# Performance work log

Hardware: AMD Instinct MI355X
Metric: run time of the kernel (lower is better)

## Reference

```python
import jax, jax.numpy as jnp
import numpy as np

B, N, MW, H, C, K = 64, 8192, 128, 8, 1024, 3
HD = C // H  # head width = 128


def setup_inputs() -> dict:
    key = jax.random.key(0)
    ks = jax.random.split(key, 16)
    s = 0.02
    return {
        "control_state": jax.random.normal(ks[0], (B, C), jnp.float32),
        "memory": jax.random.normal(ks[1], (B, N, MW), jnp.float32),
        "prev_weights": jax.nn.softmax(jax.random.normal(ks[2], (B, H, N), jnp.float32), axis=-1),
        "defaults": jax.nn.softmax(jax.random.normal(ks[3], (B, H, N), jnp.float32), axis=-1),
        "W_head": s * jax.random.normal(ks[4], (C, H * HD), jnp.float32),
        "b_head": jnp.zeros((H, HD), jnp.float32),
        "W_reset": s * jax.random.normal(ks[5], (H, HD, 1), jnp.float32),
        "b_reset": jnp.zeros((H, 1), jnp.float32),
        "W_key": s * jax.random.normal(ks[6], (H, HD, MW), jnp.float32),
        "b_key": jnp.zeros((H, MW), jnp.float32),
        "W_beta": s * jax.random.normal(ks[7], (H, HD, 1), jnp.float32),
        "b_beta": jnp.zeros((H, 1), jnp.float32),
        "W_gate": s * jax.random.normal(ks[8], (H, HD, 1), jnp.float32),
        "b_gate": jnp.zeros((H, 1), jnp.float32),
        "W_shift": s * jax.random.normal(ks[9], (H, HD, K), jnp.float32),
        "b_shift": jnp.zeros((H, K), jnp.float32),
        "W_gamma": s * jax.random.normal(ks[10], (H, HD, 1), jnp.float32),
        "b_gamma": jnp.zeros((H, 1), jnp.float32),
        "merge_w": jax.random.normal(ks[11], (H,), jnp.float32) * 0.3 + 1.0 / H,
    }


def reference(control_state, memory, prev_weights, defaults, W_head, b_head,
              W_reset, b_reset, W_key, b_key, W_beta, b_beta, W_gate, b_gate,
              W_shift, b_shift, W_gamma, b_gamma, merge_w):
    eps = 1e-8
    # head projection: [B,C] -> [B,H,HD]
    heads = (control_state @ W_head).reshape(-1, H, HD) + b_head
    # sigmoid reset gate: convex blend of prior weights with defaults
    reset_p = jax.nn.sigmoid(jnp.einsum('bhd,hdo->bho', heads, W_reset) + b_reset)  # [B,H,1]
    weights = prev_weights * (1.0 - reset_p) + defaults * reset_p
    # NTM addressing parameters (per-head linear maps)
    key_ = jnp.einsum('bhd,hdw->bhw', heads, W_key) + b_key          # [B,H,MW]
    beta = jax.nn.softplus(jnp.einsum('bhd,hdo->bho', heads, W_beta) + b_beta)   # [B,H,1]
    gate = jax.nn.sigmoid(jnp.einsum('bhd,hdo->bho', heads, W_gate) + b_gate)    # [B,H,1]
    shift = jax.nn.softmax(jnp.einsum('bhd,hdk->bhk', heads, W_shift) + b_shift, axis=-1)  # [B,H,K]
    gamma = 1.0 + jax.nn.softplus(jnp.einsum('bhd,hdo->bho', heads, W_gamma) + b_gamma)    # [B,H,1]
    # content addressing: sharpened cosine similarity softmax over memory slots
    sim = jnp.einsum('bhw,bnw->bhn', key_, memory)
    sim = sim / (jnp.linalg.norm(key_, axis=-1, keepdims=True)
                 * jnp.linalg.norm(memory, axis=-1)[:, None, :] + eps)
    content = jax.nn.softmax(beta * sim, axis=-1)                    # [B,H,N]
    # interpolate with (possibly reset) prior weights
    w_g = gate * content + (1.0 - gate) * weights
    # location addressing: circular convolution with shift kernel symmetric around 0
    w_s = sum(shift[..., j:j + 1] * jnp.roll(w_g, j - K // 2, axis=-1) for j in range(K))
    # sharpening
    w_pow = (w_s + eps) ** gamma
    new_w = w_pow / jnp.sum(w_pow, axis=-1, keepdims=True)           # [B,H,N]
    # read: per-head attention matmul against memory, then weighted head merge
    headed = jnp.einsum('bhn,bnw->bhw', new_w, memory)               # [B,H,MW]
    out = jnp.einsum('bhw,h->bw', headed, merge_w)                   # [B,MW]
    return out, new_w
```

## Files before the change

kernel.cpp:

```cpp
#include <hip/hip_runtime.h>
#include <hip/hip_bf16.h>
#include <math.h>

#define Bb 64
#define Nn 8192
#define MWw 128
#define Hh 8
#define Cc 1024
#define HDd 128
#define Kk 3

__device__ __forceinline__ float dot4(float4 a, float4 b) {
  return a.x*b.x + a.y*b.y + a.z*b.z + a.w*b.w;
}
__device__ __forceinline__ float sigmoidf_(float x) { return 1.0f / (1.0f + __expf(-x)); }
__device__ __forceinline__ float softplusf_(float x) {
  return fmaxf(x, 0.0f) + log1pf(__expf(-fabsf(x)));
}

__global__ __launch_bounds__(1024) void k_params(
    const float* __restrict__ cs, const float* __restrict__ W_head, const float* __restrict__ b_head,
    const float* __restrict__ W_reset, const float* __restrict__ b_reset,
    const float* __restrict__ W_key, const float* __restrict__ b_key,
    const float* __restrict__ W_beta, const float* __restrict__ b_beta,
    const float* __restrict__ W_gate, const float* __restrict__ b_gate,
    const float* __restrict__ W_shift, const float* __restrict__ b_shift,
    const float* __restrict__ W_gamma, const float* __restrict__ b_gamma,
    float* __restrict__ key_ws, float* __restrict__ params)
{
  int bh = blockIdx.x;
  int b = bh >> 3, h = bh & 7;
  int t = threadIdx.x;
  int d = t & 127, sl = t >> 7;
  __shared__ float red[8][128];
  __shared__ float head_s[128];
  __shared__ float key_s[128];

  const float* csb = cs + b * Cc + sl * 128;
  const float* w0 = W_head + (size_t)(sl * 128) * (Hh * HDd) + h * HDd + d;
  float acc = 0.0f;
  #pragma unroll 8
  for (int c = 0; c < 128; ++c) acc = fmaf(csb[c], w0[(size_t)c * (Hh * HDd)], acc);
  red[sl][d] = acc;
  __syncthreads();
  if (t < 128) {
    float s = b_head[h * HDd + t];
    #pragma unroll
    for (int j = 0; j < 8; ++j) s += red[j][t];
    head_s[t] = s;
  }
  __syncthreads();

  {
    const float* wk = W_key + (size_t)h * HDd * MWw + (sl * 16) * MWw + d;
    float ka = 0.0f;
    #pragma unroll
    for (int dd = 0; dd < 16; ++dd) ka = fmaf(head_s[sl * 16 + dd], wk[dd * MWw], ka);
    red[sl][d] = ka;
  }
  __syncthreads();
  if (t < 128) {
    float kv = b_key[h * MWw + t];
    #pragma unroll
    for (int j = 0; j < 8; ++j) kv += red[j][t];
    key_ws[bh * MWw + t] = kv;
    key_s[t] = kv;
  }
  __syncthreads();

  float hd = head_s[d];
  float v;
  switch (sl) {
    case 0: v = hd * W_reset[h * HDd + d]; break;
    case 1: v = hd * W_beta[h * HDd + d]; break;
    case 2: v = hd * W_gate[h * HDd + d]; break;
    case 3: v = hd * W_gamma[h * HDd + d]; break;
    case 4: v = hd * W_shift[(h * HDd + d) * Kk + 0]; break;
    case 5: v = hd * W_shift[(h * HDd + d) * Kk + 1]; break;
    case 6: v = hd * W_shift[(h * HDd + d) * Kk + 2]; break;
    default: v = key_s[d] * key_s[d]; break;
  }
  red[sl][d] = v;
  __syncthreads();
  for (int s = 64; s > 0; s >>= 1) {
    if (d < s) red[sl][d] += red[sl][d + s];
    __syncthreads();
  }
  if (t == 0) {
    float reset = sigmoidf_(red[0][0] + b_reset[h]);
    float beta  = softplusf_(red[1][0] + b_beta[h]);
    float gate  = sigmoidf_(red[2][0] + b_gate[h]);
    float gamma = 1.0f + softplusf_(red[3][0] + b_gamma[h]);
    float a0 = red[4][0] + b_shift[h * Kk + 0];
    float a1 = red[5][0] + b_shift[h * Kk + 1];
    float a2 = red[6][0] + b_shift[h * Kk + 2];
    float mx = fmaxf(a0, fmaxf(a1, a2));
    float e0 = __expf(a0 - mx), e1 = __expf(a1 - mx), e2 = __expf(a2 - mx);
    float inv = 1.0f / (e0 + e1 + e2);
    float* P = params + bh * 8;
    P[0] = reset; P[1] = beta; P[2] = gate; P[3] = gamma;
    P[4] = e0 * inv; P[5] = e1 * inv; P[6] = e2 * inv;
    P[7] = sqrtf(red[7][0]);
  }
}

__global__ __launch_bounds__(256, 2) void k_sim(
    const float* __restrict__ mem, const float* __restrict__ key_ws,
    const float* __restrict__ params, float* __restrict__ e_ws, float* __restrict__ Z)
{
  int b = blockIdx.y, chunk = blockIdx.x;
  int t = threadIdx.x;
  int lane = t & 63, wid = t >> 6;
  int sub = lane & 7, rid = lane >> 3;
  __shared__ float4 keys[8][32];
  __shared__ float betas[8], knorms[8];
  __shared__ float e_s[8][520];
  if (t < 8) { betas[t] = params[(b * 8 + t) * 8 + 1]; knorms[t] = params[(b * 8 + t) * 8 + 7]; }
  {
    int h = t >> 5, q = t & 31;
    keys[h][q] = ((const float4*)key_ws)[(b * 8 + h) * 32 + q];
  }
  __syncthreads();

  float4 kreg[8][4];
  #pragma unroll
  for (int h2 = 0; h2 < 8; ++h2) {
    kreg[h2][0] = keys[h2][sub];
    kreg[h2][1] = keys[h2][sub + 8];
    kreg[h2][2] = keys[h2][sub + 16];
    kreg[h2][3] = keys[h2][sub + 24];
  }

  const float4* m4 = (const float4*)mem + (size_t)b * Nn * 32;
  float beta = betas[sub], kn = knorms[sub];
  float zloc = 0.0f;
  int n0 = chunk * 512;

  #pragma unroll 1
  for (int itr = 0; itr < 8; ++itr) {
    int nb = n0 + itr * 64 + wid * 16 + rid;
    float4 m[2][4];
    float nrm[2];
    float acc[2][8];
    #pragma unroll
    for (int r = 0; r < 2; ++r) {
      const float4* rp = m4 + (size_t)(nb + r * 8) * 32 + sub;
      m[r][0] = rp[0]; m[r][1] = rp[8]; m[r][2] = rp[16]; m[r][3] = rp[24];
    }
    #pragma unroll
    for (int r = 0; r < 2; ++r) {
      nrm[r] = dot4(m[r][0], m[r][0]) + dot4(m[r][1], m[r][1])
             + dot4(m[r][2], m[r][2]) + dot4(m[r][3], m[r][3]);
      #pragma unroll
      for (int h2 = 0; h2 < 8; ++h2) {
        acc[r][h2] = dot4(m[r][0], kreg[h2][0]) + dot4(m[r][1], kreg[h2][1])
                   + dot4(m[r][2], kreg[h2][2]) + dot4(m[r][3], kreg[h2][3]);
      }
    }
    #pragma unroll
    for (int r = 0; r < 2; ++r) {
      float* a = acc[r];
      bool h1 = (sub & 1) != 0;
      float v40 = (h1 ? a[1] : a[0]) + __shfl_xor(h1 ? a[0] : a[1], 1, 64);
      float v41 = (h1 ? a[3] : a[2]) + __shfl_xor(h1 ? a[2] : a[3], 1, 64);
      float v42 = (h1 ? a[5] : a[4]) + __shfl_xor(h1 ? a[4] : a[5], 1, 64);
      float v43 = (h1 ? a[7] : a[6]) + __shfl_xor(h1 ? a[6] : a[7], 1, 64);
      bool h2b = (sub & 2) != 0;
      float v20 = (h2b ? v41 : v40) + __shfl_xor(h2b ? v40 : v41, 2, 64);
      float v21 = (h2b ? v43 : v42) + __shfl_xor(h2b ? v42 : v43, 2, 64);
      bool h4 = (sub & 4) != 0;
      float dsum = (h4 ? v21 : v20) + __shfl_xor(h4 ? v20 : v21, 4, 64);
      float nr = nrm[r];
      nr += __shfl_xor(nr, 1, 64);
      nr += __shfl_xor(nr, 2, 64);
      nr += __shfl_xor(nr, 4, 64);
      float s = beta * dsum / (kn * sqrtf(nr) + 1e-8f);
      float e = __expf(s - beta);
      e_s[sub][(nb + r * 8) - n0] = e;
      zloc += e;
    }
  }
  zloc += __shfl_xor(zloc, 8, 64);
  zloc += __shfl_xor(zloc, 16, 64);
  zloc += __shfl_xor(zloc, 32, 64);
  if (lane < 8) atomicAdd(&Z[b * 8 + lane], zloc);
  __syncthreads();

  #pragma unroll
  for (int j = 0; j < 4; ++j) {
    int idx = j * 256 + t;
    int h = idx >> 7, q = idx & 127;
    float4 v = *(const float4*)&e_s[h][q * 4];
    ((float4*)(e_ws + (size_t)(b * 8 + h) * Nn + n0))[q] = v;
  }
}

__global__ __launch_bounds__(256) void k_conv(
    const float* __restrict__ e_ws, const float* __restrict__ prev, const float* __restrict__ defw,
    const float* __restrict__ params, const float* __restrict__ Z,
    float* __restrict__ wp, float* __restrict__ S)
{
  int chunk = blockIdx.x, h = blockIdx.y, b = blockIdx.z;
  int bh = b * 8 + h, t = threadIdx.x;
  __shared__ float wg[2052];
  const float* P = params + bh * 8;
  float reset = P[0], gate = P[2], gamma = P[3], s0 = P[4], s1 = P[5], s2 = P[6];
  float invZg = gate / Z[bh];
  float om = 1.0f - gate, omr = 1.0f - reset;
  size_t base = (size_t)bh * Nn;
  int n0 = chunk * 2048;

  const float4* e4p = (const float4*)(e_ws + base + n0);
  const float4* p4p = (const float4*)(prev + base + n0);
  const float4* d4p = (const float4*)(defw + base + n0);
  #pragma unroll
  for (int it = 0; it < 2; ++it) {
    int idx4 = it * 256 + t;
    float4 e = e4p[idx4], pv = p4p[idx4], dv = d4p[idx4];
    float4 w;
    w.x = invZg * e.x + om * (pv.x * omr + dv.x * reset);
    w.y = invZg * e.y + om * (pv.y * omr + dv.y * reset);
    w.z = invZg * e.z + om * (pv.z * omr + dv.z * reset);
    w.w = invZg * e.w + om * (pv.w * omr + dv.w * reset);
    *(float4*)&wg[idx4 * 4] = w;
  }
  if (t < 2) {
    int n = (t == 0) ? ((n0 + Nn - 1) & (Nn - 1)) : ((n0 + 2048) & (Nn - 1));
    float e = e_ws[base + n], pv = prev[base + n], dv = defw[base + n];
    wg[2048 + t] = invZg * e + om * (pv * omr + dv * reset);
  }
  __syncthreads();

  float sacc = 0.0f;
  float4* wp4 = (float4*)(wp + base + n0);
  #pragma unroll
  for (int it = 0; it < 2; ++it) {
    int idx4 = it * 256 + t;
    int l = idx4 * 4;
    float4 c = *(const float4*)&wg[l];
    float left  = (l == 0)        ? wg[2048] : wg[l - 1];
    float right = (l + 4 == 2048) ? wg[2049] : wg[l + 4];
    float4 wsv;
    wsv.x = s0 * c.y   + s1 * c.x + s2 * left;
    wsv.y = s0 * c.z   + s1 * c.y + s2 * c.x;
    wsv.z = s0 * c.w   + s1 * c.z + s2 * c.y;
    wsv.w = s0 * right + s1 * c.w + s2 * c.z;
    float4 o;
    o.x = __expf(gamma * __logf(wsv.x + 1e-8f));
    o.y = __expf(gamma * __logf(wsv.y + 1e-8f));
    o.z = __expf(gamma * __logf(wsv.z + 1e-8f));
    o.w = __expf(gamma * __logf(wsv.w + 1e-8f));
    wp4[idx4] = o;
    sacc += o.x + o.y + o.z + o.w;
  }
  sacc += __shfl_xor(sacc, 1, 64);
  sacc += __shfl_xor(sacc, 2, 64);
  sacc += __shfl_xor(sacc, 4, 64);
  sacc += __shfl_xor(sacc, 8, 64);
  sacc += __shfl_xor(sacc, 16, 64);
  sacc += __shfl_xor(sacc, 32, 64);
  __shared__ float sred[4];
  if ((t & 63) == 0) sred[t >> 6] = sacc;
  __syncthreads();
  if (t == 0) atomicAdd(&S[bh], sred[0] + sred[1] + sred[2] + sred[3]);
}

__global__ __launch_bounds__(256) void k_readnorm(
    const float* __restrict__ mem, float* __restrict__ wp, const float* __restrict__ S,
    const float* __restrict__ merge_w, float* __restrict__ out)
{
  int b = blockIdx.y; int n0 = blockIdx.x * 512; int t = threadIdx.x;
  __shared__ float kh[8], invS_s[8];
  __shared__ float coef_s[512];
  __shared__ float4 red4[256];
  if (t < 8) {
    float s = S[b * 8 + t];
    invS_s[t] = 1.0f / s;
    kh[t] = merge_w[t] / s;
  }
  __syncthreads();

  #pragma unroll
  for (int ii = 0; ii < 2; ++ii) {
    int nl = ii * 256 + t;
    float cf = 0.0f;
    #pragma unroll
    for (int h = 0; h < 8; ++h) {
      size_t idx = (size_t)(b * 8 + h) * Nn + n0 + nl;
      float v = wp[idx];
      wp[idx] = v * invS_s[h];
      cf = fmaf(kh[h], v, cf);
    }
    coef_s[nl] = cf;
  }
  __syncthreads();

  int w4 = t & 31, rg = t >> 5;
  const float4* m4 = (const float4*)mem + (size_t)b * Nn * 32;
  float4 acc = make_float4(0.0f, 0.0f, 0.0f, 0.0f);
  #pragma unroll 4
  for (int it = 0; it < 64; ++it) {
    int nl = it * 8 + rg;
    float c = coef_s[nl];
    float4 m = m4[(size_t)(n0 + nl) * 32 + w4];
    acc.x = fmaf(c, m.x, acc.x);
    acc.y = fmaf(c, m.y, acc.y);
    acc.z = fmaf(c, m.z, acc.z);
    acc.w = fmaf(c, m.w, acc.w);
  }
  red4[t] = acc;
  __syncthreads();
  if (t < 32) {
    float4 s = red4[t];
    #pragma unroll
    for (int j = 1; j < 8; ++j) {
      float4 o = red4[t + 32 * j];
      s.x += o.x; s.y += o.y; s.z += o.z; s.w += o.w;
    }
    atomicAdd(&out[b * MWw + t * 4 + 0], s.x);
    atomicAdd(&out[b * MWw + t * 4 + 1], s.y);
    atomicAdd(&out[b * MWw + t * 4 + 2], s.z);
    atomicAdd(&out[b * MWw + t * 4 + 3], s.w);
  }
}

extern "C" void kernel_launch(void* const* d_in, const int* in_sizes, int n_in,
                              void* d_out, int out_size, void* d_ws, size_t ws_size,
                              hipStream_t stream)
{
  const float* cs      = (const float*)d_in[0];
  const float* mem     = (const float*)d_in[1];
  const float* prev    = (const float*)d_in[2];
  const float* defw    = (const float*)d_in[3];
  const float* W_head  = (const float*)d_in[4];
  const float* b_head  = (const float*)d_in[5];
  const float* W_reset = (const float*)d_in[6];
  const float* b_reset = (const float*)d_in[7];
  const float* W_key   = (const float*)d_in[8];
  const float* b_key   = (const float*)d_in[9];
  const float* W_beta  = (const float*)d_in[10];
  const float* b_beta  = (const float*)d_in[11];
  const float* W_gate  = (const float*)d_in[12];
  const float* b_gate  = (const float*)d_in[13];
  const float* W_shift = (const float*)d_in[14];
  const float* b_shift = (const float*)d_in[15];
  const float* W_gamma = (const float*)d_in[16];
  const float* b_gamma = (const float*)d_in[17];
  const float* merge_w = (const float*)d_in[18];

  float* out  = (float*)d_out;
  float* neww = out + Bb * MWw;

  float* ws_f   = (float*)d_ws;
  float* key_ws = ws_f;
  float* params = ws_f + 65536;
  float* Zacc   = ws_f + 69632;
  float* Sacc   = ws_f + 70144;
  float* e_ws   = ws_f + 70656;

  hipMemsetAsync(Zacc, 0, 1024 * sizeof(float), stream);
  hipMemsetAsync(out, 0, Bb * MWw * sizeof(float), stream);

  k_params<<<dim3(Bb * Hh), dim3(1024), 0, stream>>>(
      cs, W_head, b_head, W_reset, b_reset, W_key, b_key, W_beta, b_beta,
      W_gate, b_gate, W_shift, b_shift, W_gamma, b_gamma, key_ws, params);
  k_sim<<<dim3(16, Bb), dim3(256), 0, stream>>>(mem, key_ws, params, e_ws, Zacc);
  k_conv<<<dim3(4, Hh, Bb), dim3(256), 0, stream>>>(e_ws, prev, defw, params, Zacc, neww, Sacc);
  k_readnorm<<<dim3(16, Bb), dim3(256), 0, stream>>>(mem, neww, Sacc, merge_w, out);
}
```

Measured before the change: 501.1 us.

## Fold memsets into params kernel, shuffle reductions, vectorize readnorm rescale

Removes the two hipMemsetAsync calls by having block 0 of k_params zero the Z accumulator and output buffer. It also replaces the shared-memory tree reduction in k_params with wavefront shuffles, and rewrites the k_readnorm weight rescale to use float4 loads and stores split across two head groups. This is meant to cut launch overhead and barrier count and to widen memory accesses, at the cost of one extra shared-memory reduction step.

```diff
diff --git a/kernel.cpp b/kernel.cpp
--- a/kernel.cpp
+++ b/kernel.cpp
@@ -26,7 +26,8 @@
     const float* __restrict__ W_gate, const float* __restrict__ b_gate,
     const float* __restrict__ W_shift, const float* __restrict__ b_shift,
     const float* __restrict__ W_gamma, const float* __restrict__ b_gamma,
-    float* __restrict__ key_ws, float* __restrict__ params)
+    float* __restrict__ key_ws, float* __restrict__ params,
+    float* __restrict__ zs, float* __restrict__ outp)
 {
   int bh = blockIdx.x;
   int b = bh >> 3, h = bh & 7;
@@ -35,6 +36,13 @@
   __shared__ float red[8][128];
   __shared__ float head_s[128];
   __shared__ float key_s[128];
+  __shared__ float wred[16];
+
+  if (bh == 0) {
+    zs[t] = 0.0f;
+    #pragma unroll
+    for (int j = 0; j < 8; ++j) outp[j * 1024 + t] = 0.0f;
+  }
 
   const float* csb = cs + b * Cc + sl * 128;
   const float* w0 = W_head + (size_t)(sl * 128) * (Hh * HDd) + h * HDd + d;
@@ -80,27 +88,37 @@
     case 6: v = hd * W_shift[(h * HDd + d) * Kk + 2]; break;
     default: v = key_s[d] * key_s[d]; break;
   }
-  red[sl][d] = v;
-  __syncthreads();
-  for (int s = 64; s > 0; s >>= 1) {
-    if (d < s) red[sl][d] += red[sl][d + s];
-    __syncthreads();
-  }
+  v += __shfl_xor(v, 1, 64);
+  v += __shfl_xor(v, 2, 64);
+  v += __shfl_xor(v, 4, 64);
+  v += __shfl_xor(v, 8, 64);
+  v += __shfl_xor(v, 16, 64);
+  v += __shfl_xor(v, 32, 64);
+  if ((t & 63) == 0) wred[t >> 6] = v;
+  __syncthreads();
   if (t == 0) {
-    float reset = sigmoidf_(red[0][0] + b_reset[h]);
-    float beta  = softplusf_(red[1][0] + b_beta[h]);
-    float gate  = sigmoidf_(red[2][0] + b_gate[h]);
-    float gamma = 1.0f + softplusf_(red[3][0] + b_gamma[h]);
-    float a0 = red[4][0] + b_shift[h * Kk + 0];
-    float a1 = red[5][0] + b_shift[h * Kk + 1];
-    float a2 = red[6][0] + b_shift[h * Kk + 2];
+    float r0 = wred[0]  + wred[1];
+    float r1 = wred[2]  + wred[3];
+    float r2 = wred[4]  + wred[5];
+    float r3 = wred[6]  + wred[7];
+    float r4 = wred[8]  + wred[9];
+    float r5 = wred[10] + wred[11];
+    float r6 = wred[12] + wred[13];
+    float r7 = wred[14] + wred[15];
+    float reset = sigmoidf_(r0 + b_reset[h]);
+    float beta  = softplusf_(r1 + b_beta[h]);
+    float gate  = sigmoidf_(r2 + b_gate[h]);
+    float gamma = 1.0f + softplusf_(r3 + b_gamma[h]);
+    float a0 = r4 + b_shift[h * Kk + 0];
+    float a1 = r5 + b_shift[h * Kk + 1];
+    float a2 = r6 + b_shift[h * Kk + 2];
     float mx = fmaxf(a0, fmaxf(a1, a2));
     float e0 = __expf(a0 - mx), e1 = __expf(a1 - mx), e2 = __expf(a2 - mx);
     float inv = 1.0f / (e0 + e1 + e2);
     float* P = params + bh * 8;
     P[0] = reset; P[1] = beta; P[2] = gate; P[3] = gamma;
     P[4] = e0 * inv; P[5] = e1 * inv; P[6] = e2 * inv;
-    P[7] = sqrtf(red[7][0]);
+    P[7] = sqrtf(r7);
   }
 }
 
@@ -280,18 +298,29 @@
   }
   __syncthreads();
 
-  #pragma unroll
-  for (int ii = 0; ii < 2; ++ii) {
-    int nl = ii * 256 + t;
-    float cf = 0.0f;
-    #pragma unroll
-    for (int h = 0; h < 8; ++h) {
-      size_t idx = (size_t)(b * 8 + h) * Nn + n0 + nl;
-      float v = wp[idx];
-      wp[idx] = v * invS_s[h];
-      cf = fmaf(kh[h], v, cf);
-    }
-    coef_s[nl] = cf;
+  int col = t & 127, grp = t >> 7;
+  float4 cf = make_float4(0.0f, 0.0f, 0.0f, 0.0f);
+  #pragma unroll
+  for (int hh = 0; hh < 4; ++hh) {
+    int h = grp * 4 + hh;
+    float4* wph = (float4*)(wp + (size_t)(b * 8 + h) * Nn + n0);
+    float4 v = wph[col];
+    float is = invS_s[h], k = kh[h];
+    float4 o;
+    o.x = v.x * is; o.y = v.y * is; o.z = v.z * is; o.w = v.w * is;
+    wph[col] = o;
+    cf.x = fmaf(k, v.x, cf.x);
+    cf.y = fmaf(k, v.y, cf.y);
+    cf.z = fmaf(k, v.z, cf.z);
+    cf.w = fmaf(k, v.w, cf.w);
+  }
+  red4[grp * 128 + col] = cf;
+  __syncthreads();
+  if (t < 128) {
+    float4 a = red4[t], c = red4[128 + t];
+    float4 s4;
+    s4.x = a.x + c.x; s4.y = a.y + c.y; s4.z = a.z + c.z; s4.w = a.w + c.w;
+    *(float4*)&coef_s[t * 4] = s4;
   }
   __syncthreads();
 
@@ -358,12 +387,10 @@
   float* Sacc   = ws_f + 70144;
   float* e_ws   = ws_f + 70656;
 
-  hipMemsetAsync(Zacc, 0, 1024 * sizeof(float), stream);
-  hipMemsetAsync(out, 0, Bb * MWw * sizeof(float), stream);
-
   k_params<<<dim3(Bb * Hh), dim3(1024), 0, stream>>>(
       cs, W_head, b_head, W_reset, b_reset, W_key, b_key, W_beta, b_beta,
-      W_gate, b_gate, W_shift, b_shift, W_gamma, b_gamma, key_ws, params);
+      W_gate, b_gate, W_shift, b_shift, W_gamma, b_gamma, key_ws, params,
+      Zacc, out);
   k_sim<<<dim3(16, Bb), dim3(256), 0, stream>>>(mem, key_ws, params, e_ws, Zacc);
   k_conv<<<dim3(4, Hh, Bb), dim3(256), 0, stream>>>(e_ws, prev, defw, params, Zacc, neww, Sacc);
   k_readnorm<<<dim3(16, Bb), dim3(256), 0, stream>>>(mem, neww, Sacc, merge_w, out);
```

Result: no change. 495.1 us (-1.2%).
